# Optimization experiments

Hardware: AMD Instinct MI355X
Metric: run time of the kernel (lower is better)

## Reference

```python
import jax, jax.numpy as jnp
import numpy as np

MAX_PATH_DISTANCE = 512  # embedding table rows
B, T, Q = 64, 1024, 128
E = 200000  # cached (node1,node2) pairs per graph


def setup_inputs() -> dict:
    key = jax.random.key(0)
    k1, k2, k3, k4 = jax.random.split(key, 4)
    x = jax.random.normal(k1, (B, T, Q), dtype=jnp.float32)
    path_distance_map = jax.random.randint(k2, (B, E), 0, MAX_PATH_DISTANCE, dtype=jnp.int32)
    edge_index_map = jax.random.randint(k3, (B, E, 2), 0, T, dtype=jnp.int32)
    # learned parameter: nn.Embedding(max_path_distance, 1) weight
    weight = jax.random.normal(k4, (MAX_PATH_DISTANCE, 1), dtype=jnp.float32)
    return {"x": x, "weight": weight,
            "path_distance_map": path_distance_map,
            "edge_index_map": edge_index_map}


def reference(x, weight, path_distance_map, edge_index_map):
    Bb, Tt, _ = x.shape
    # initialize every pair with the 'non-existent path' encoding = last embedding row
    out = jnp.broadcast_to(weight[-1, 0], (Bb, Tt, Tt))
    # gather: per-pair distance embedding, shape (B, E)
    emb = weight[path_distance_map, 0]
    # scatter into (batch, node1, node2) slots
    b_idx = jnp.arange(Bb, dtype=edge_index_map.dtype)[:, None]  # (B,1)
    out = out.at[b_idx, edge_index_map[..., 0], edge_index_map[..., 1]].set(emb)
    return out
```

## Files before the change

### kernel.cpp

```cpp
#include <hip/hip_runtime.h>


#define BB 64
#define TT 1024
#define EE 200000
#define MAXD 512
#define GRP 8
#define NG  (TT / GRP)
#define CAPR 4096
#define CPB 2048
#define EPT 8

__global__ void __launch_bounds__(256)
bin_kernel(const int* __restrict__ pdm,
           const int* __restrict__ eim,
           int* __restrict__ gcnt,
           int2* __restrict__ grecs) {
    __shared__ int hist[NG], prefix[NG], resv[NG];
    __shared__ int wsum[2];
    __shared__ int2 rec[CPB];
    __shared__ int dst[CPB];
    const int tid = threadIdx.x;
    const int b = blockIdx.y;
    const int e0 = blockIdx.x * CPB + tid * EPT;

    int dvals[EPT]; int2 nvals[EPT]; int nv;
    const int* pb = pdm + (size_t)b * EE;
    const int2* ebp = ((const int2*)eim) + (size_t)b * EE;
    if (e0 + EPT <= EE) {
        const int4* p4 = (const int4*)(pb + e0);
        int4 pA = p4[0], pB = p4[1];
        const int4* e4 = (const int4*)(ebp + e0);
        int4 eA = e4[0], eB = e4[1], eC = e4[2], eD = e4[3];
        dvals[0]=pA.x; dvals[1]=pA.y; dvals[2]=pA.z; dvals[3]=pA.w;
        dvals[4]=pB.x; dvals[5]=pB.y; dvals[6]=pB.z; dvals[7]=pB.w;
        nvals[0]=make_int2(eA.x,eA.y); nvals[1]=make_int2(eA.z,eA.w);
        nvals[2]=make_int2(eB.x,eB.y); nvals[3]=make_int2(eB.z,eB.w);
        nvals[4]=make_int2(eC.x,eC.y); nvals[5]=make_int2(eC.z,eC.w);
        nvals[6]=make_int2(eD.x,eD.y); nvals[7]=make_int2(eD.z,eD.w);
        nv = EPT;
    } else {
        nv = EE - e0; if (nv < 0) nv = 0; if (nv > EPT) nv = EPT;
        #pragma unroll
        for (int k = 0; k < EPT; ++k)
            if (k < nv) { dvals[k] = pb[e0 + k]; nvals[k] = ebp[e0 + k]; }
    }

    for (int i = tid; i < NG; i += 256) hist[i] = 0;
    __syncthreads();

    int g[EPT], rk[EPT];
    #pragma unroll
    for (int k = 0; k < EPT; ++k) {
        if (k < nv) {
            g[k] = nvals[k].x >> 3;
            rk[k] = atomicAdd(&hist[g[k]], 1);
        }
    }
    __syncthreads();

    if (tid < NG) {
        int v = hist[tid], inc = v;
        #pragma unroll
        for (int off = 1; off < 64; off <<= 1) {
            int t = __shfl_up(inc, off);
            if ((tid & 63) >= off) inc += t;
        }
        if ((tid & 63) == 63) wsum[tid >> 6] = inc;
        prefix[tid] = inc - v;
        resv[tid] = atomicAdd(&gcnt[b * NG + tid], v);
    }
    __syncthreads();
    if (tid >= 64 && tid < NG) prefix[tid] += wsum[0];
    __syncthreads();

    #pragma unroll
    for (int k = 0; k < EPT; ++k) {
        if (k < nv) {
            int e = e0 + k;
            int lp = prefix[g[k]] + rk[k];
            rec[lp] = make_int2(((nvals[k].x & (GRP - 1)) << 10) | nvals[k].y,
                                (e << 9) | dvals[k]);
            int gp = resv[g[k]] + rk[k];
            dst[lp] = (gp < CAPR) ? (((b * NG + g[k]) << 12) | gp) : -1;
        }
    }
    __syncthreads();

    int total = EE - blockIdx.x * CPB;
    if (total > CPB) total = CPB;
    for (int j = tid; j < total; j += 256) {
        int dd = dst[j];
        if (dd >= 0)
            grecs[((size_t)(dd >> 12) << 12) | (dd & (CAPR - 1))] = rec[j];
    }
}

__global__ void __launch_bounds__(512)
resolve_kernel(const float* __restrict__ w,
               const int* __restrict__ gcnt,
               float* __restrict__ out) {
    __shared__ int tile[GRP * TT];
    __shared__ float sw[MAXD];
    const int tid = threadIdx.x;
    const int q = blockIdx.x;

    int c = gcnt[q]; if (c > CAPR) c = CAPR;
    const int4* recs4 = (const int4*)(((const int2*)out) + ((size_t)q * CAPR));
    int4 pre[4];
    #pragma unroll
    for (int k = 0; k < 4; ++k) {
        int i4 = tid + k * 512;
        if (2 * i4 < c) pre[k] = recs4[i4];
    }

    for (int i = tid; i < MAXD; i += 512) sw[i] = w[i];
    int4* t4 = (int4*)tile;
    for (int i = tid; i < GRP * TT / 4; i += 512)
        t4[i] = make_int4(-1, -1, -1, -1);
    __syncthreads();

    #pragma unroll
    for (int k = 0; k < 4; ++k) {
        int i4 = tid + k * 512;
        int r0 = 2 * i4, r1 = 2 * i4 + 1;
        if (r0 < c) atomicMax(&tile[pre[k].x], pre[k].y);
        if (r1 < c) atomicMax(&tile[pre[k].z], pre[k].w);
    }
    __syncthreads();

    float4* o4 = (float4*)(out + (size_t)q * (GRP * TT));
    for (int i = tid; i < GRP * TT / 4; i += 512) {
        int4 v = t4[i];
        float4 r;
        r.x = sw[v.x < 0 ? (MAXD - 1) : (v.x & (MAXD - 1))];
        r.y = sw[v.y < 0 ? (MAXD - 1) : (v.y & (MAXD - 1))];
        r.z = sw[v.z < 0 ? (MAXD - 1) : (v.z & (MAXD - 1))];
        r.w = sw[v.w < 0 ? (MAXD - 1) : (v.w & (MAXD - 1))];
        o4[i] = r;
    }
}


__global__ void __launch_bounds__(256)
scatter_max_kernel(const int* __restrict__ pdm,
                   const int* __restrict__ eim,
                   int* __restrict__ outi) {
    int e = blockIdx.x * blockDim.x + threadIdx.x;
    int b = blockIdx.y;
    if (e >= EE) return;
    int d = pdm[(size_t)b * EE + e];
    int2 n = ((const int2*)eim)[(size_t)b * EE + e];
    atomicMax(&outi[((size_t)b * TT + (size_t)n.x) * TT + (size_t)n.y],
              (e << 9) | d);
}

__global__ void __launch_bounds__(256)
finalize_kernel(const float* __restrict__ w, float* __restrict__ out, size_t n4) {
    const size_t stride = (size_t)gridDim.x * blockDim.x;
    int4* pi = (int4*)out;
    float4* pf = (float4*)out;
    for (size_t i = (size_t)blockIdx.x * blockDim.x + threadIdx.x; i < n4; i += stride) {
        int4 v = pi[i];
        float4 r;
        r.x = w[v.x < 0 ? (MAXD - 1) : (v.x & (MAXD - 1))];
        r.y = w[v.y < 0 ? (MAXD - 1) : (v.y & (MAXD - 1))];
        r.z = w[v.z < 0 ? (MAXD - 1) : (v.z & (MAXD - 1))];
        r.w = w[v.w < 0 ? (MAXD - 1) : (v.w & (MAXD - 1))];
        pf[i] = r;
    }
}

extern "C" void kernel_launch(void* const* d_in, const int* in_sizes, int n_in,
                              void* d_out, int out_size, void* d_ws, size_t ws_size,
                              hipStream_t stream) {
    const float* w   = (const float*)d_in[1];
    const int*   pdm = (const int*)d_in[2];
    const int*   eim = (const int*)d_in[3];
    float* out = (float*)d_out;

    const size_t cnt_bytes = (size_t)BB * NG * sizeof(int);

    if (ws_size >= cnt_bytes) {
        (void)hipMemsetAsync(d_ws, 0, cnt_bytes, stream);
        dim3 bgrid((EE + CPB - 1) / CPB, BB);
        bin_kernel<<<bgrid, 256, 0, stream>>>(pdm, eim, (int*)d_ws, (int2*)d_out);
        resolve_kernel<<<BB * NG, 512, 0, stream>>>(w, (const int*)d_ws, out);
    } else {
        (void)hipMemsetAsync(d_out, 0xFF, (size_t)out_size * sizeof(float), stream);
        dim3 sgrid((EE + 255) / 256, BB);
        scatter_max_kernel<<<sgrid, 256, 0, stream>>>(pdm, eim, (int*)d_out);
        finalize_kernel<<<2048, 256, 0, stream>>>(w, out, (size_t)out_size / 4);
    }
}
```

Before: 123.7 us.

## Use per-wave histograms and larger bin chunks, drop dst array in binning

The binning kernel now handles 4096 edges per block with 512 threads, halving the number of blocks and of global counter atomics per group. The shared histogram is split into one copy per wave, which reduces LDS atomic contention; the per-wave offsets are folded into the prefix. The separate dst array is removed: the group id is packed into the upper bits of the record and the global destination is recomputed at write-out. This adds LDS usage and a serial per-wave scan, and may lower occupancy.

```diff
diff --git a/kernel.cpp b/kernel.cpp
--- a/kernel.cpp
+++ b/kernel.cpp
@@ -7,20 +7,23 @@
 #define MAXD 512
 #define GRP 8
 #define NG  (TT / GRP)
+#define NQ  (BB * NG)
 #define CAPR 4096
-#define CPB 2048
+#define CPB 4096
 #define EPT 8
-
-__global__ void __launch_bounds__(256)
+#define BTHR 512
+
+__global__ void __launch_bounds__(512)
 bin_kernel(const int* __restrict__ pdm,
            const int* __restrict__ eim,
            int* __restrict__ gcnt,
            int2* __restrict__ grecs) {
-    __shared__ int hist[NG], prefix[NG], resv[NG];
+    __shared__ int hist[8][NG];
+    __shared__ int prefix[NG], resv[NG];
     __shared__ int wsum[2];
     __shared__ int2 rec[CPB];
-    __shared__ int dst[CPB];
     const int tid = threadIdx.x;
+    const int wave = tid >> 6;
     const int b = blockIdx.y;
     const int e0 = blockIdx.x * CPB + tid * EPT;
 
@@ -46,7 +49,7 @@
             if (k < nv) { dvals[k] = pb[e0 + k]; nvals[k] = ebp[e0 + k]; }
     }
 
-    for (int i = tid; i < NG; i += 256) hist[i] = 0;
+    for (int i = tid; i < 8 * NG; i += BTHR) ((int*)hist)[i] = 0;
     __syncthreads();
 
     int g[EPT], rk[EPT];
@@ -54,13 +57,18 @@
     for (int k = 0; k < EPT; ++k) {
         if (k < nv) {
             g[k] = nvals[k].x >> 3;
-            rk[k] = atomicAdd(&hist[g[k]], 1);
+            rk[k] = atomicAdd(&hist[wave][g[k]], 1);
         }
     }
     __syncthreads();
 
     if (tid < NG) {
-        int v = hist[tid], inc = v;
+        int run = 0;
+        #pragma unroll
+        for (int w = 0; w < 8; ++w) {
+            int h = hist[w][tid]; hist[w][tid] = run; run += h;
+        }
+        int v = run, inc = run;
         #pragma unroll
         for (int off = 1; off < 64; off <<= 1) {
             int t = __shfl_up(inc, off);
@@ -77,22 +85,23 @@
     #pragma unroll
     for (int k = 0; k < EPT; ++k) {
         if (k < nv) {
-            int e = e0 + k;
-            int lp = prefix[g[k]] + rk[k];
-            rec[lp] = make_int2(((nvals[k].x & (GRP - 1)) << 10) | nvals[k].y,
-                                (e << 9) | dvals[k]);
-            int gp = resv[g[k]] + rk[k];
-            dst[lp] = (gp < CAPR) ? (((b * NG + g[k]) << 12) | gp) : -1;
+            int lp = prefix[g[k]] + hist[wave][g[k]] + rk[k];
+            rec[lp] = make_int2((g[k] << 13) |
+                                ((nvals[k].x & (GRP - 1)) << 10) | nvals[k].y,
+                                ((e0 + k) << 9) | dvals[k]);
         }
     }
     __syncthreads();
 
     int total = EE - blockIdx.x * CPB;
     if (total > CPB) total = CPB;
-    for (int j = tid; j < total; j += 256) {
-        int dd = dst[j];
-        if (dd >= 0)
-            grecs[((size_t)(dd >> 12) << 12) | (dd & (CAPR - 1))] = rec[j];
+    for (int j = tid; j < total; j += BTHR) {
+        int2 r = rec[j];
+        int gg = r.x >> 13;
+        int gp = resv[gg] + (j - prefix[gg]);
+        if (gp < CAPR)
+            grecs[(size_t)(b * NG + gg) * CAPR + gp] =
+                make_int2(r.x & 0x1FFF, r.y);
     }
 }
 
@@ -179,13 +188,13 @@
     const int*   eim = (const int*)d_in[3];
     float* out = (float*)d_out;
 
-    const size_t cnt_bytes = (size_t)BB * NG * sizeof(int);
+    const size_t cnt_bytes = (size_t)NQ * sizeof(int);
 
     if (ws_size >= cnt_bytes) {
         (void)hipMemsetAsync(d_ws, 0, cnt_bytes, stream);
         dim3 bgrid((EE + CPB - 1) / CPB, BB);
-        bin_kernel<<<bgrid, 256, 0, stream>>>(pdm, eim, (int*)d_ws, (int2*)d_out);
-        resolve_kernel<<<BB * NG, 512, 0, stream>>>(w, (const int*)d_ws, out);
+        bin_kernel<<<bgrid, BTHR, 0, stream>>>(pdm, eim, (int*)d_ws, (int2*)d_out);
+        resolve_kernel<<<NQ, 512, 0, stream>>>(w, (const int*)d_ws, out);
     } else {
         (void)hipMemsetAsync(d_out, 0xFF, (size_t)out_size * sizeof(float), stream);
         dim3 sgrid((EE + 255) / 256, BB);
```

New measurement: 124.6 us. About the same (+0.7%).
